# Optimization experiments

Hardware: AMD Instinct MI355X
Metric: run time of the kernel (lower is better)

The kernel has to match this reference:

```python
import jax, jax.numpy as jnp
import numpy as np

# Static config (matches init_kwargs)
B, F, CIN, COUT, H, W = 2, 8, 16, 32, 128, 128
RB, GB = 1, 1                 # refer_band, guard_band_dop (range_doppler)
KH, KW = 2 * (RB + GB), 4     # PeakConv kernel
N = KH * KW                   # ring samples per pixel (16)
LEAK, EPS = 0.01, 1e-5


def _ring_offsets(rb, gb):
    """Peripheral-reference-frame ring offsets, in the exact order of _gen_prf_grid."""
    r = rb + gb
    hp = 2 * r + 1
    xs, ys = np.meshgrid(np.arange(-r, r + 1), np.arange(-r, r + 1), indexing='ij')
    def ring(a):
        top = a[0:rb]
        rgt = a[rb:hp - 2 * rb + 1, hp - rb:hp]
        dwn = a[hp - rb:hp]
        lft = a[rb:hp - 2 * rb + 1, 0:rb]
        return np.concatenate([top.ravel(), rgt.ravel(), dwn.ravel(), lft.ravel()])
    return ring(xs), ring(ys)

_OX, _OY = _ring_offsets(RB, GB)  # each (N,)


def _peak_conv(x, Wk, bk):
    # x: (b, c, h, w)
    bsz, c, h, w = x.shape
    pad = RB + GB
    xp = jnp.pad(x, ((0, 0), (0, 0), (pad, pad), (pad, pad)))
    ii = jnp.arange(h)[:, None, None] + pad + jnp.asarray(_OX)[None, None, :]  # (h,1,N)
    jj = jnp.arange(w)[None, :, None] + pad + jnp.asarray(_OY)[None, None, :]  # (1,w,N)
    x_r = xp[:, :, ii, jj]                       # (b,c,h,w,N) ring gather
    diff = x[..., None] - x_r                    # center minus ring (x_c - x_r)
    diff = diff.reshape(bsz, c, h, w, KH, KW)    # matches _reshape_x_prf tiling
    # conv with kernel (KH,KW), stride (KH,KW) over tiled map == per-pixel contraction
    return jnp.einsum('bchwgj,ocgj->bohw', diff, Wk) + bk[None, :, None, None]


def _bn_leaky(x, gamma, beta):
    mu = x.mean(axis=(0, 2, 3), keepdims=True)
    var = x.var(axis=(0, 2, 3), keepdims=True)  # biased, as torch BN uses for normalization
    y = (x - mu) * jax.lax.rsqrt(var + EPS)
    y = y * gamma[None, :, None, None] + beta[None, :, None, None]
    return jnp.where(y >= 0, y, LEAK * y)


def setup_inputs() -> dict:
    key = jax.random.key(0)
    ks = jax.random.split(key, 5)
    return {
        'x':  jax.random.normal(ks[0], (B, CIN, F, H, W), dtype=jnp.float32),
        'W1': jax.random.normal(ks[1], (COUT, CIN, KH, KW), dtype=jnp.float32) * 0.05,
        'b1': jax.random.normal(ks[2], (COUT,), dtype=jnp.float32) * 0.05,
        'g1': jnp.ones((COUT,), jnp.float32),
        'be1': jnp.zeros((COUT,), jnp.float32),
        'W2': jax.random.normal(ks[3], (COUT, COUT, KH, KW), dtype=jnp.float32) * 0.05,
        'b2': jax.random.normal(ks[4], (COUT,), dtype=jnp.float32) * 0.05,
        'g2': jnp.ones((COUT,), jnp.float32),
        'be2': jnp.zeros((COUT,), jnp.float32),
    }


def reference(x, W1, b1, g1, be1, W2, b2, g2, be2):
    # (B, CIN, F, H, W) -> permute -> flatten to (B*F, CIN, H, W)
    xx = jnp.transpose(x, (0, 2, 1, 3, 4)).reshape(B * F, CIN, H, W)
    y = _bn_leaky(_peak_conv(xx, W1, b1), g1, be1)
    y = _bn_leaky(_peak_conv(y, W2, b2), g2, be2)
    # NOTE: original does .view(B, C, F, h, w) on a (B*F, C, h, w) contiguous
    # tensor — a raw reinterpretation, reproduced exactly by this reshape.
    y = y.reshape(B, COUT, F, H, W)
    return y.mean(axis=2, keepdims=True)  # AvgPool3d((F,1,1)) -> (B, COUT, 1, H, W)
```

## Files before the change

### kernel.cpp

```cpp
#include <hip/hip_runtime.h>

using short8 = __attribute__((ext_vector_type(8))) short;
using sh4    = __attribute__((ext_vector_type(4))) short;
using f32x4  = __attribute__((ext_vector_type(4))) float;
typedef unsigned short ushort_t;

constexpr int BB = 2, FF = 8, CIN = 16, COUT = 32, HH = 128, WW = 128;
constexpr int HW   = HH * WW;
constexpr int NIMG = BB * FF;
constexpr int TIL = 16, HALO = 2, LP = 20, NPX = 400;
constexpr int NSLOT = 1024;
constexpr int WFN = 17 * 2 * 512;

__device__ const int DOFF[17] = { -42,-41,-40,-39,-38, -18,2,22, 38,39,40,41,42, -22,-2,18, 0 };

__device__ __forceinline__ float leaky(float v) { return v >= 0.f ? v : 0.01f * v; }
__device__ __forceinline__ ushort_t f2bf(float f) {
    unsigned u = __builtin_bit_cast(unsigned, f);
    u = (u + 0x7FFFu + ((u >> 16) & 1u)) >> 16;
    return (ushort_t)u;
}
__device__ __forceinline__ float bf2f(ushort_t h) {
    unsigned u = ((unsigned)h) << 16;
    return __builtin_bit_cast(float, u);
}

__global__ __launch_bounds__(256)
void prep_weights(const float* __restrict__ W1, const float* __restrict__ W2,
                  ushort_t* __restrict__ Wf1, ushort_t* __restrict__ Wf2)
{
    int which = blockIdx.y;
    const float* W = which ? W2 : W1;
    ushort_t* Wf   = which ? Wf2 : Wf1;
    int ci         = which ? COUT : CIN;

    int idx = blockIdx.x * 256 + threadIdx.x;
    int j  = idx & 7;
    int l  = (idx >> 3) & 63;
    int oh = (idx >> 9) & 1;
    int n  = idx >> 10;
    int oc = oh * 16 + (l & 15);
    int k  = ((l >> 4) << 3) + j;
    int c  = which ? k : (k & 15);
    const float* wp = W + ((size_t)oc * ci + c) * 16;
    float v;
    if (n < 16) v = -wp[n];
    else { v = 0.f; for (int q = 0; q < 16; ++q) v += wp[q]; }
    Wf[idx] = f2bf(v);
}

template <int MODE>
__global__ __launch_bounds__(256)
void peak_conv_mfma(const float* __restrict__ inf, const ushort_t* __restrict__ inh,
                    const ushort_t* __restrict__ Wf,
                    const float* __restrict__ bk, const float* __restrict__ prm,
                    ushort_t* __restrict__ outp, float* __restrict__ P)
{
    __shared__ __align__(16) ushort_t lds[NPX * 32];
    __shared__ float redS[4][COUT], redQ[4][COUT];

    const int tid    = threadIdx.x;
    const int tileid = blockIdx.x;
    const int img    = blockIdx.y;
    const int tx     = (tileid & 7) * TIL;
    const int ty     = (tileid >> 3) * TIL;
    const int lane   = tid & 63;
    const int wid    = tid >> 6;
    const int rxl    = lane & 15;
    const int cq     = lane >> 4;

    if (MODE == 0) {
#pragma unroll
        for (int e = 0; e < 4; ++e) {
            int task = e * 256 + tid;
            if (task < 800) {
                int h  = task >= 400 ? 1 : 0;
                int p  = task - h * 400;
                int ry = p / LP, rx = p - ry * LP;
                int gh = ty + ry - HALO, gw = tx + rx - HALO;
                bool ok = (unsigned)gh < (unsigned)HH && (unsigned)gw < (unsigned)WW;
                int ghc = min(max(gh, 0), HH - 1), gwc = min(max(gw, 0), WW - 1);
                const float* base = inf + (((size_t)(img >> 3) * CIN + 8 * h) * FF + (img & 7)) * HW
                                       + ghc * WW + gwc;
                short8 hi8, lo8;
#pragma unroll
                for (int cc = 0; cc < 8; ++cc) {
                    float v = base[(size_t)cc * FF * HW];
                    v = ok ? v : 0.f;
                    ushort_t hi = f2bf(v);
                    hi8[cc] = (short)hi;
                    lo8[cc] = (short)f2bf(v - bf2f(hi));
                }
                int swz = (p & 3) ^ ((p >> 2) & 3);
                *(short8*)&lds[p * 32 + 8 * (h ^ swz)]       = hi8;
                *(short8*)&lds[p * 32 + 8 * ((2 + h) ^ swz)] = lo8;
            }
        }
    } else {
#pragma unroll
        for (int e = 0; e < 7; ++e) {
            int task = e * 256 + tid;
            if (task < 1600) {
                int g  = task & 3, p = task >> 2;
                int ry = p / LP, rx = p - ry * LP;
                int gh = ty + ry - HALO, gw = tx + rx - HALO;
                bool ok = (unsigned)gh < (unsigned)HH && (unsigned)gw < (unsigned)WW;
                int ghc = min(max(gh, 0), HH - 1), gwc = min(max(gw, 0), WW - 1);
                const ushort_t* px = inh + ((size_t)img * HW + ghc * WW + gwc) * 32 + 8 * g;
                short8 raw = *(const short8*)px;
                short8 hv;
#pragma unroll
                for (int jj = 0; jj < 8; ++jj) {
                    int c = 8 * g + jj;
                    float v = bf2f((ushort_t)raw[jj]);
                    v = leaky(fmaf(prm[c], v, prm[COUT + c]));
                    hv[jj] = (short)f2bf(ok ? v : 0.f);
                }
                int swz = (p & 3) ^ ((p >> 2) & 3);
                *(short8*)&lds[p * 32 + 8 * (g ^ swz)] = hv;
            }
        }
    }
    __syncthreads();

    f32x4 acc[4][2];
#pragma unroll
    for (int ng = 0; ng < 4; ++ng)
#pragma unroll
        for (int oh = 0; oh < 2; ++oh) acc[ng][oh] = f32x4{0.f, 0.f, 0.f, 0.f};

    int q0[4];
#pragma unroll
    for (int ng = 0; ng < 4; ++ng) q0[ng] = (wid * 4 + ng + HALO) * LP + (rxl + HALO);

    const ushort_t* wl = Wf + (size_t)lane * 8;

#pragma unroll 1
    for (int n = 0; n < 17; ++n) {
        short8 A0 = *(const short8*)(wl + (size_t)(n * 2 + 0) * 512);
        short8 A1 = *(const short8*)(wl + (size_t)(n * 2 + 1) * 512);
        int dof = DOFF[n];
#pragma unroll
        for (int ng = 0; ng < 4; ++ng) {
            int p   = q0[ng] + dof;
            int swz = (p & 3) ^ ((p >> 2) & 3);
            short8 Bv = *(const short8*)&lds[p * 32 + 8 * (cq ^ swz)];
            acc[ng][0] = __builtin_amdgcn_mfma_f32_16x16x32_bf16(A0, Bv, acc[ng][0], 0, 0, 0);
            acc[ng][1] = __builtin_amdgcn_mfma_f32_16x16x32_bf16(A1, Bv, acc[ng][1], 0, 0, 0);
        }
    }

    float bias_[2][4];
#pragma unroll
    for (int oh = 0; oh < 2; ++oh)
#pragma unroll
        for (int rr = 0; rr < 4; ++rr) bias_[oh][rr] = bk[oh * 16 + cq * 4 + rr];

    float ssum[2][4], ssq[2][4];
#pragma unroll
    for (int oh = 0; oh < 2; ++oh)
#pragma unroll
        for (int rr = 0; rr < 4; ++rr) { ssum[oh][rr] = 0.f; ssq[oh][rr] = 0.f; }

#pragma unroll
    for (int ng = 0; ng < 4; ++ng) {
        int gh = ty + wid * 4 + ng, gw = tx + rxl;
        size_t pxb = ((size_t)img * HW + gh * WW + gw) * 32;
#pragma unroll
        for (int oh = 0; oh < 2; ++oh) {
            sh4 sv;
#pragma unroll
            for (int rr = 0; rr < 4; ++rr) {
                float v = acc[ng][oh][rr] + bias_[oh][rr];
                sv[rr] = (short)f2bf(v);
                ssum[oh][rr] += v;
                ssq[oh][rr]   = fmaf(v, v, ssq[oh][rr]);
            }
            *(sh4*)&outp[pxb + oh * 16 + cq * 4] = sv;
        }
    }

#pragma unroll
    for (int oh = 0; oh < 2; ++oh)
#pragma unroll
        for (int rr = 0; rr < 4; ++rr) {
            float s = ssum[oh][rr], q = ssq[oh][rr];
#pragma unroll
            for (int m = 1; m < 16; m <<= 1) { s += __shfl_xor(s, m); q += __shfl_xor(q, m); }
            if (rxl == 0) {
                redS[wid][oh * 16 + cq * 4 + rr] = s;
                redQ[wid][oh * 16 + cq * 4 + rr] = q;
            }
        }
    __syncthreads();

    const int slot = img * 64 + tileid;
    if (tid < COUT) {
        float s = redS[0][tid] + redS[1][tid] + redS[2][tid] + redS[3][tid];
        P[(size_t)tid * NSLOT + slot] = s;
    } else if (tid < 2 * COUT) {
        int oc = tid - COUT;
        float q = redQ[0][oc] + redQ[1][oc] + redQ[2][oc] + redQ[3][oc];
        P[(size_t)COUT * NSLOT + (size_t)oc * NSLOT + slot] = q;
    }
}

__global__ __launch_bounds__(256)
void bn_stats(const float* __restrict__ P, const float* __restrict__ gamma,
              const float* __restrict__ beta, float* __restrict__ prm)
{
    __shared__ float rs[256], rq[256];
    const int c = blockIdx.x, tid = threadIdx.x;
    const float* Ps = P + (size_t)c * NSLOT;
    const float* Pq = P + (size_t)COUT * NSLOT + (size_t)c * NSLOT;
    rs[tid] = Ps[tid] + Ps[tid + 256] + Ps[tid + 512] + Ps[tid + 768];
    rq[tid] = Pq[tid] + Pq[tid + 256] + Pq[tid + 512] + Pq[tid + 768];
    __syncthreads();
    for (int s = 128; s > 0; s >>= 1) {
        if (tid < s) { rs[tid] += rs[tid + s]; rq[tid] += rq[tid + s]; }
        __syncthreads();
    }
    if (tid == 0) {
        const float n = (float)(NIMG * HW);
        float mu  = rs[0] / n;
        float var = rq[0] / n - mu * mu;
        float a   = gamma[c] * rsqrtf(var + 1e-5f);
        prm[c]        = a;
        prm[COUT + c] = beta[c] - mu * a;
    }
}

__global__ __launch_bounds__(256)
void finalize(const ushort_t* __restrict__ t2, const float* __restrict__ prm,
              float* __restrict__ outp)
{
    int gid  = blockIdx.x * 256 + threadIdx.x;
    int p    = gid & (HW - 1);
    int rest = gid >> 14;
    int o    = rest & 31;
    int b    = rest >> 5;
    int img  = b * 8 + (o >> 2);
    int cb   = (o & 3) * 8;
    const ushort_t* px = t2 + ((size_t)img * HW + p) * 32 + cb;
    short8 raw = *(const short8*)px;
    float s = 0.f;
#pragma unroll
    for (int j = 0; j < 8; ++j) {
        int c = cb + j;
        float v = bf2f((ushort_t)raw[j]);
        s += leaky(fmaf(prm[c], v, prm[COUT + c]));
    }
    outp[gid] = 0.125f * s;
}

extern "C" void kernel_launch(void* const* d_in, const int* in_sizes, int n_in,
                              void* d_out, int out_size, void* d_ws, size_t ws_size,
                              hipStream_t stream)
{
    const float* x   = (const float*)d_in[0];
    const float* W1  = (const float*)d_in[1];
    const float* b1  = (const float*)d_in[2];
    const float* g1  = (const float*)d_in[3];
    const float* be1 = (const float*)d_in[4];
    const float* W2  = (const float*)d_in[5];
    const float* b2  = (const float*)d_in[6];
    const float* g2  = (const float*)d_in[7];
    const float* be2 = (const float*)d_in[8];
    float* out = (float*)d_out;

    const size_t TSZH = (size_t)NIMG * HW * 32;
    ushort_t* t1   = (ushort_t*)d_ws;
    ushort_t* t2   = t1 + TSZH;
    float*    P    = (float*)(t2 + TSZH);
    float*    prm1 = P + 2 * COUT * NSLOT;
    float*    prm2 = prm1 + 2 * COUT;
    ushort_t* Wf1  = (ushort_t*)(prm2 + 2 * COUT);
    ushort_t* Wf2  = Wf1 + WFN;

    dim3 pg(WFN / 256, 2);
    prep_weights<<<pg, 256, 0, stream>>>(W1, W2, Wf1, Wf2);

    dim3 cg(64, NIMG);
    peak_conv_mfma<0><<<cg, 256, 0, stream>>>(x,  nullptr, Wf1, b1, nullptr, t1, P);
    bn_stats<<<COUT, 256, 0, stream>>>(P, g1, be1, prm1);
    peak_conv_mfma<1><<<cg, 256, 0, stream>>>(nullptr, t1, Wf2, b2, prm1,   t2, P);
    bn_stats<<<COUT, 256, 0, stream>>>(P, g2, be2, prm2);
    finalize<<<(BB * COUT * HW) / 256, 256, 0, stream>>>(t2, prm2, out);
}
```

Before: 64.18 us.

## Fuse whole pipeline into one cooperative kernel with grid syncs

Replaces the six-launch sequence (weight prep, two convs, two BN-stat reductions, finalize) with a single cooperative kernel that uses grid-wide syncs between phases. Each block does the BN statistics reduction redundantly, and the second conv's accumulators stay in registers for the final BN+leaky+frame-average, so the t2 intermediate is never written or re-read. Partial sums are stored interleaved as (sum, sumsq) pairs. The aim is to remove launch gaps and one round trip of the intermediate through memory, at the cost of grid-sync latency, redundant per-block reductions, and needing all 1024 blocks co-resident. A fallback multi-kernel path with BN reduction folded into the consumers is kept for when cooperative launch is unavailable.

```diff
diff --git a/kernel.cpp b/kernel.cpp
--- a/kernel.cpp
+++ b/kernel.cpp
@@ -1,8 +1,12 @@
 #include <hip/hip_runtime.h>
+#include <hip/hip_cooperative_groups.h>
+
+namespace cg = cooperative_groups;
 
 using short8 = __attribute__((ext_vector_type(8))) short;
 using sh4    = __attribute__((ext_vector_type(4))) short;
 using f32x4  = __attribute__((ext_vector_type(4))) float;
+using f32x2  = __attribute__((ext_vector_type(2))) float;
 typedef unsigned short ushort_t;
 
 constexpr int BB = 2, FF = 8, CIN = 16, COUT = 32, HH = 128, WW = 128;
@@ -25,6 +29,265 @@
     return __builtin_bit_cast(float, u);
 }
 
+__device__ __forceinline__ void bn_reduce(const float* __restrict__ Pv,
+                                          const float* __restrict__ gamma,
+                                          const float* __restrict__ beta,
+                                          float* sprm, int tid)
+{
+    int c = tid >> 3, l8 = tid & 7;
+    const f32x2* base = (const f32x2*)(Pv + (size_t)c * 2 * NSLOT);
+    float s = 0.f, q = 0.f;
+    for (int k = 0; k < 128; ++k) {
+        f32x2 v = base[l8 + (k << 3)];
+        s += v[0]; q += v[1];
+    }
+#pragma unroll
+    for (int m = 1; m < 8; m <<= 1) { s += __shfl_xor(s, m); q += __shfl_xor(q, m); }
+    if (l8 == 0) {
+        const float n = (float)(NIMG * HW);
+        float mu  = s / n;
+        float var = q / n - mu * mu;
+        float a   = gamma[c] * rsqrtf(var + 1e-5f);
+        sprm[c]        = a;
+        sprm[COUT + c] = beta[c] - mu * a;
+    }
+}
+
+template <int MODE, bool STORE>
+__device__ __forceinline__ void conv_phase(
+    const float* __restrict__ inf, const ushort_t* __restrict__ inh,
+    const ushort_t* __restrict__ Wf, const float* __restrict__ bk,
+    const float* sprm, ushort_t* __restrict__ tout, float* __restrict__ Pv,
+    ushort_t* lds, float (*redS)[COUT], float (*redQ)[COUT],
+    int img, int tileid, int tid, f32x4 (&acc)[4][2])
+{
+    const int tx   = (tileid & 7) * TIL;
+    const int ty   = (tileid >> 3) * TIL;
+    const int lane = tid & 63;
+    const int wid  = tid >> 6;
+    const int rxl  = lane & 15;
+    const int cq   = lane >> 4;
+
+    if (MODE == 0) {
+#pragma unroll
+        for (int e = 0; e < 4; ++e) {
+            int task = e * 256 + tid;
+            if (task < 800) {
+                int h  = task >= 400 ? 1 : 0;
+                int p  = task - h * 400;
+                int ry = p / LP, rx = p - ry * LP;
+                int gh = ty + ry - HALO, gw = tx + rx - HALO;
+                bool ok = (unsigned)gh < (unsigned)HH && (unsigned)gw < (unsigned)WW;
+                int ghc = min(max(gh, 0), HH - 1), gwc = min(max(gw, 0), WW - 1);
+                const float* base = inf + (((size_t)(img >> 3) * CIN + 8 * h) * FF + (img & 7)) * HW
+                                       + ghc * WW + gwc;
+                short8 hi8, lo8;
+#pragma unroll
+                for (int cc = 0; cc < 8; ++cc) {
+                    float v = base[(size_t)cc * FF * HW];
+                    v = ok ? v : 0.f;
+                    ushort_t hi = f2bf(v);
+                    hi8[cc] = (short)hi;
+                    lo8[cc] = (short)f2bf(v - bf2f(hi));
+                }
+                int swz = (p & 3) ^ ((p >> 2) & 3);
+                *(short8*)&lds[p * 32 + 8 * (h ^ swz)]       = hi8;
+                *(short8*)&lds[p * 32 + 8 * ((2 + h) ^ swz)] = lo8;
+            }
+        }
+    } else {
+#pragma unroll
+        for (int e = 0; e < 7; ++e) {
+            int task = e * 256 + tid;
+            if (task < 1600) {
+                int g  = task & 3, p = task >> 2;
+                int ry = p / LP, rx = p - ry * LP;
+                int gh = ty + ry - HALO, gw = tx + rx - HALO;
+                bool ok = (unsigned)gh < (unsigned)HH && (unsigned)gw < (unsigned)WW;
+                int ghc = min(max(gh, 0), HH - 1), gwc = min(max(gw, 0), WW - 1);
+                const ushort_t* px = inh + ((size_t)img * HW + ghc * WW + gwc) * 32 + 8 * g;
+                short8 raw = *(const short8*)px;
+                short8 hv;
+#pragma unroll
+                for (int jj = 0; jj < 8; ++jj) {
+                    int c = 8 * g + jj;
+                    float v = bf2f((ushort_t)raw[jj]);
+                    v = leaky(fmaf(sprm[c], v, sprm[COUT + c]));
+                    hv[jj] = (short)f2bf(ok ? v : 0.f);
+                }
+                int swz = (p & 3) ^ ((p >> 2) & 3);
+                *(short8*)&lds[p * 32 + 8 * (g ^ swz)] = hv;
+            }
+        }
+    }
+    __syncthreads();
+
+#pragma unroll
+    for (int ng = 0; ng < 4; ++ng)
+#pragma unroll
+        for (int oh = 0; oh < 2; ++oh) acc[ng][oh] = f32x4{0.f, 0.f, 0.f, 0.f};
+
+    int q0[4];
+#pragma unroll
+    for (int ng = 0; ng < 4; ++ng) q0[ng] = (wid * 4 + ng + HALO) * LP + (rxl + HALO);
+
+    const ushort_t* wl = Wf + (size_t)lane * 8;
+
+#pragma unroll 1
+    for (int n = 0; n < 17; ++n) {
+        short8 A0 = *(const short8*)(wl + (size_t)(n * 2 + 0) * 512);
+        short8 A1 = *(const short8*)(wl + (size_t)(n * 2 + 1) * 512);
+        int dof = DOFF[n];
+#pragma unroll
+        for (int ng = 0; ng < 4; ++ng) {
+            int p   = q0[ng] + dof;
+            int swz = (p & 3) ^ ((p >> 2) & 3);
+            short8 Bv = *(const short8*)&lds[p * 32 + 8 * (cq ^ swz)];
+            acc[ng][0] = __builtin_amdgcn_mfma_f32_16x16x32_bf16(A0, Bv, acc[ng][0], 0, 0, 0);
+            acc[ng][1] = __builtin_amdgcn_mfma_f32_16x16x32_bf16(A1, Bv, acc[ng][1], 0, 0, 0);
+        }
+    }
+
+    float ssum[2][4], ssq[2][4];
+#pragma unroll
+    for (int oh = 0; oh < 2; ++oh)
+#pragma unroll
+        for (int rr = 0; rr < 4; ++rr) {
+            float b = bk[oh * 16 + cq * 4 + rr];
+#pragma unroll
+            for (int ng = 0; ng < 4; ++ng) acc[ng][oh][rr] += b;
+            ssum[oh][rr] = 0.f; ssq[oh][rr] = 0.f;
+        }
+
+#pragma unroll
+    for (int ng = 0; ng < 4; ++ng) {
+        int gh = ty + wid * 4 + ng, gw = tx + rxl;
+        size_t pxb = ((size_t)img * HW + gh * WW + gw) * 32;
+#pragma unroll
+        for (int oh = 0; oh < 2; ++oh) {
+            sh4 sv;
+#pragma unroll
+            for (int rr = 0; rr < 4; ++rr) {
+                float v = acc[ng][oh][rr];
+                sv[rr] = (short)f2bf(v);
+                ssum[oh][rr] += v;
+                ssq[oh][rr]   = fmaf(v, v, ssq[oh][rr]);
+            }
+            if (STORE) *(sh4*)&tout[pxb + oh * 16 + cq * 4] = sv;
+        }
+    }
+
+#pragma unroll
+    for (int oh = 0; oh < 2; ++oh)
+#pragma unroll
+        for (int rr = 0; rr < 4; ++rr) {
+            float s = ssum[oh][rr], q = ssq[oh][rr];
+#pragma unroll
+            for (int m = 1; m < 16; m <<= 1) { s += __shfl_xor(s, m); q += __shfl_xor(q, m); }
+            if (rxl == 0) {
+                redS[wid][oh * 16 + cq * 4 + rr] = s;
+                redQ[wid][oh * 16 + cq * 4 + rr] = q;
+            }
+        }
+    __syncthreads();
+
+    const int slot = img * 64 + tileid;
+    if (tid < COUT) {
+        float s = redS[0][tid] + redS[1][tid] + redS[2][tid] + redS[3][tid];
+        float q = redQ[0][tid] + redQ[1][tid] + redQ[2][tid] + redQ[3][tid];
+        ((f32x2*)Pv)[(size_t)tid * NSLOT + slot] = f32x2{s, q};
+    }
+}
+
+__global__ __launch_bounds__(256, 4)
+void fused(const float* __restrict__ x,  const float* __restrict__ W1,
+           const float* __restrict__ b1, const float* __restrict__ g1,
+           const float* __restrict__ be1, const float* __restrict__ W2,
+           const float* __restrict__ b2, const float* __restrict__ g2,
+           const float* __restrict__ be2, float* __restrict__ out,
+           ushort_t* __restrict__ t1, float* __restrict__ Pv1,
+           float* __restrict__ Pv2, ushort_t* __restrict__ Wf1,
+           ushort_t* __restrict__ Wf2)
+{
+    cg::grid_group grid = cg::this_grid();
+
+    __shared__ __align__(16) ushort_t lds[NPX * 32];
+    __shared__ float redS[4][COUT], redQ[4][COUT];
+    __shared__ float sprm[2 * COUT];
+
+    const int tid    = threadIdx.x;
+    const int tileid = blockIdx.x;
+    const int img    = blockIdx.y;
+    const int bid    = img * 64 + tileid;
+
+    if (bid < 2 * WFN / 256) {
+        int idx   = bid * 256 + tid;
+        int which = idx >= WFN;
+        int sub   = which ? idx - WFN : idx;
+        const float* W = which ? W2 : W1;
+        ushort_t* Wf   = which ? Wf2 : Wf1;
+        int ci         = which ? COUT : CIN;
+        int j  = sub & 7;
+        int l  = (sub >> 3) & 63;
+        int oh = (sub >> 9) & 1;
+        int n  = sub >> 10;
+        int oc = oh * 16 + (l & 15);
+        int k  = ((l >> 4) << 3) + j;
+        int c  = which ? k : (k & 15);
+        const float* wp = W + ((size_t)oc * ci + c) * 16;
+        float v;
+        if (n < 16) v = -wp[n];
+        else { v = 0.f; for (int q = 0; q < 16; ++q) v += wp[q]; }
+        Wf[sub] = f2bf(v);
+    }
+    __threadfence();
+    grid.sync();
+    __threadfence();
+
+    f32x4 acc[4][2];
+    conv_phase<0, true>(x, nullptr, Wf1, b1, nullptr, t1, Pv1,
+                        lds, redS, redQ, img, tileid, tid, acc);
+    __threadfence();
+    grid.sync();
+    __threadfence();
+
+    bn_reduce(Pv1, g1, be1, sprm, tid);
+    __syncthreads();
+
+    conv_phase<1, false>(nullptr, t1, Wf2, b2, sprm, nullptr, Pv2,
+                         lds, redS, redQ, img, tileid, tid, acc);
+    __threadfence();
+    grid.sync();
+    __threadfence();
+
+    bn_reduce(Pv2, g2, be2, sprm, tid);
+    __syncthreads();
+
+    const int lane = tid & 63, wid = tid >> 6;
+    const int rxl  = lane & 15, cq = lane >> 4;
+    const int tx   = (tileid & 7) * TIL, ty = (tileid >> 3) * TIL;
+    const int b    = img >> 3;
+    const int obase = (img & 7) * 4;
+#pragma unroll
+    for (int ng = 0; ng < 4; ++ng) {
+        int gh = ty + wid * 4 + ng, gw = tx + rxl;
+#pragma unroll
+        for (int oh = 0; oh < 2; ++oh) {
+            float s = 0.f;
+#pragma unroll
+            for (int rr = 0; rr < 4; ++rr) {
+                int c = oh * 16 + cq * 4 + rr;
+                s += leaky(fmaf(sprm[c], acc[ng][oh][rr], sprm[COUT + c]));
+            }
+            s += __shfl_xor(s, 16);
+            if ((cq & 1) == 0) {
+                int o = obase + oh * 2 + (cq >> 1);
+                out[((size_t)b * COUT + o) * HW + gh * WW + gw] = 0.125f * s;
+            }
+        }
+    }
+}
+
 __global__ __launch_bounds__(256)
 void prep_weights(const float* __restrict__ W1, const float* __restrict__ W2,
                   ushort_t* __restrict__ Wf1, ushort_t* __restrict__ Wf2)
@@ -33,7 +296,6 @@
     const float* W = which ? W2 : W1;
     ushort_t* Wf   = which ? Wf2 : Wf1;
     int ci         = which ? COUT : CIN;
-
     int idx = blockIdx.x * 256 + threadIdx.x;
     int j  = idx & 7;
     int l  = (idx >> 3) & 63;
@@ -49,208 +311,63 @@
     Wf[idx] = f2bf(v);
 }
 
-template <int MODE>
 __global__ __launch_bounds__(256)
-void peak_conv_mfma(const float* __restrict__ inf, const ushort_t* __restrict__ inh,
-                    const ushort_t* __restrict__ Wf,
-                    const float* __restrict__ bk, const float* __restrict__ prm,
-                    ushort_t* __restrict__ outp, float* __restrict__ P)
+void conv1_k(const float* __restrict__ x, const ushort_t* __restrict__ Wf1,
+             const float* __restrict__ b1, ushort_t* __restrict__ t1,
+             float* __restrict__ Pv1)
 {
     __shared__ __align__(16) ushort_t lds[NPX * 32];
     __shared__ float redS[4][COUT], redQ[4][COUT];
-
-    const int tid    = threadIdx.x;
-    const int tileid = blockIdx.x;
-    const int img    = blockIdx.y;
-    const int tx     = (tileid & 7) * TIL;
-    const int ty     = (tileid >> 3) * TIL;
-    const int lane   = tid & 63;
-    const int wid    = tid >> 6;
-    const int rxl    = lane & 15;
-    const int cq     = lane >> 4;
-
-    if (MODE == 0) {
-#pragma unroll
-        for (int e = 0; e < 4; ++e) {
-            int task = e * 256 + tid;
-            if (task < 800) {
-                int h  = task >= 400 ? 1 : 0;
-                int p  = task - h * 400;
-                int ry = p / LP, rx = p - ry * LP;
-                int gh = ty + ry - HALO, gw = tx + rx - HALO;
-                bool ok = (unsigned)gh < (unsigned)HH && (unsigned)gw < (unsigned)WW;
-                int ghc = min(max(gh, 0), HH - 1), gwc = min(max(gw, 0), WW - 1);
-                const float* base = inf + (((size_t)(img >> 3) * CIN + 8 * h) * FF + (img & 7)) * HW
-                                       + ghc * WW + gwc;
-                short8 hi8, lo8;
-#pragma unroll
-                for (int cc = 0; cc < 8; ++cc) {
-                    float v = base[(size_t)cc * FF * HW];
-                    v = ok ? v : 0.f;
-                    ushort_t hi = f2bf(v);
-                    hi8[cc] = (short)hi;
-                    lo8[cc] = (short)f2bf(v - bf2f(hi));
-                }
-                int swz = (p & 3) ^ ((p >> 2) & 3);
-                *(short8*)&lds[p * 32 + 8 * (h ^ swz)]       = hi8;
-                *(short8*)&lds[p * 32 + 8 * ((2 + h) ^ swz)] = lo8;
-            }
-        }
-    } else {
-#pragma unroll
-        for (int e = 0; e < 7; ++e) {
-            int task = e * 256 + tid;
-            if (task < 1600) {
-                int g  = task & 3, p = task >> 2;
-                int ry = p / LP, rx = p - ry * LP;
-                int gh = ty + ry - HALO, gw = tx + rx - HALO;
-                bool ok = (unsigned)gh < (unsigned)HH && (unsigned)gw < (unsigned)WW;
-                int ghc = min(max(gh, 0), HH - 1), gwc = min(max(gw, 0), WW - 1);
-                const ushort_t* px = inh + ((size_t)img * HW + ghc * WW + gwc) * 32 + 8 * g;
-                short8 raw = *(const short8*)px;
-                short8 hv;
-#pragma unroll
-                for (int jj = 0; jj < 8; ++jj) {
-                    int c = 8 * g + jj;
-                    float v = bf2f((ushort_t)raw[jj]);
-                    v = leaky(fmaf(prm[c], v, prm[COUT + c]));
-                    hv[jj] = (short)f2bf(ok ? v : 0.f);
-                }
-                int swz = (p & 3) ^ ((p >> 2) & 3);
-                *(short8*)&lds[p * 32 + 8 * (g ^ swz)] = hv;
-            }
-        }
-    }
-    __syncthreads();
-
     f32x4 acc[4][2];
-#pragma unroll
-    for (int ng = 0; ng < 4; ++ng)
-#pragma unroll
-        for (int oh = 0; oh < 2; ++oh) acc[ng][oh] = f32x4{0.f, 0.f, 0.f, 0.f};
-
-    int q0[4];
-#pragma unroll
-    for (int ng = 0; ng < 4; ++ng) q0[ng] = (wid * 4 + ng + HALO) * LP + (rxl + HALO);
-
-    const ushort_t* wl = Wf + (size_t)lane * 8;
-
-#pragma unroll 1
-    for (int n = 0; n < 17; ++n) {
-        short8 A0 = *(const short8*)(wl + (size_t)(n * 2 + 0) * 512);
-        short8 A1 = *(const short8*)(wl + (size_t)(n * 2 + 1) * 512);
-        int dof = DOFF[n];
-#pragma unroll
-        for (int ng = 0; ng < 4; ++ng) {
-            int p   = q0[ng] + dof;
-            int swz = (p & 3) ^ ((p >> 2) & 3);
-            short8 Bv = *(const short8*)&lds[p * 32 + 8 * (cq ^ swz)];
-            acc[ng][0] = __builtin_amdgcn_mfma_f32_16x16x32_bf16(A0, Bv, acc[ng][0], 0, 0, 0);
-            acc[ng][1] = __builtin_amdgcn_mfma_f32_16x16x32_bf16(A1, Bv, acc[ng][1], 0, 0, 0);
-        }
-    }
-
-    float bias_[2][4];
-#pragma unroll
-    for (int oh = 0; oh < 2; ++oh)
-#pragma unroll
-        for (int rr = 0; rr < 4; ++rr) bias_[oh][rr] = bk[oh * 16 + cq * 4 + rr];
-
-    float ssum[2][4], ssq[2][4];
-#pragma unroll
-    for (int oh = 0; oh < 2; ++oh)
-#pragma unroll
-        for (int rr = 0; rr < 4; ++rr) { ssum[oh][rr] = 0.f; ssq[oh][rr] = 0.f; }
-
-#pragma unroll
-    for (int ng = 0; ng < 4; ++ng) {
-        int gh = ty + wid * 4 + ng, gw = tx + rxl;
-        size_t pxb = ((size_t)img * HW + gh * WW + gw) * 32;
-#pragma unroll
-        for (int oh = 0; oh < 2; ++oh) {
-            sh4 sv;
-#pragma unroll
-            for (int rr = 0; rr < 4; ++rr) {
-                float v = acc[ng][oh][rr] + bias_[oh][rr];
-                sv[rr] = (short)f2bf(v);
-                ssum[oh][rr] += v;
-                ssq[oh][rr]   = fmaf(v, v, ssq[oh][rr]);
-            }
-            *(sh4*)&outp[pxb + oh * 16 + cq * 4] = sv;
-        }
-    }
-
-#pragma unroll
-    for (int oh = 0; oh < 2; ++oh)
-#pragma unroll
-        for (int rr = 0; rr < 4; ++rr) {
-            float s = ssum[oh][rr], q = ssq[oh][rr];
-#pragma unroll
-            for (int m = 1; m < 16; m <<= 1) { s += __shfl_xor(s, m); q += __shfl_xor(q, m); }
-            if (rxl == 0) {
-                redS[wid][oh * 16 + cq * 4 + rr] = s;
-                redQ[wid][oh * 16 + cq * 4 + rr] = q;
-            }
-        }
-    __syncthreads();
-
-    const int slot = img * 64 + tileid;
-    if (tid < COUT) {
-        float s = redS[0][tid] + redS[1][tid] + redS[2][tid] + redS[3][tid];
-        P[(size_t)tid * NSLOT + slot] = s;
-    } else if (tid < 2 * COUT) {
-        int oc = tid - COUT;
-        float q = redQ[0][oc] + redQ[1][oc] + redQ[2][oc] + redQ[3][oc];
-        P[(size_t)COUT * NSLOT + (size_t)oc * NSLOT + slot] = q;
-    }
+    conv_phase<0, true>(x, nullptr, Wf1, b1, nullptr, t1, Pv1,
+                        lds, redS, redQ, blockIdx.y, blockIdx.x, threadIdx.x, acc);
 }
 
 __global__ __launch_bounds__(256)
-void bn_stats(const float* __restrict__ P, const float* __restrict__ gamma,
-              const float* __restrict__ beta, float* __restrict__ prm)
-{
-    __shared__ float rs[256], rq[256];
-    const int c = blockIdx.x, tid = threadIdx.x;
-    const float* Ps = P + (size_t)c * NSLOT;
-    const float* Pq = P + (size_t)COUT * NSLOT + (size_t)c * NSLOT;
-    rs[tid] = Ps[tid] + Ps[tid + 256] + Ps[tid + 512] + Ps[tid + 768];
-    rq[tid] = Pq[tid] + Pq[tid + 256] + Pq[tid + 512] + Pq[tid + 768];
-    __syncthreads();
-    for (int s = 128; s > 0; s >>= 1) {
-        if (tid < s) { rs[tid] += rs[tid + s]; rq[tid] += rq[tid + s]; }
-        __syncthreads();
-    }
-    if (tid == 0) {
-        const float n = (float)(NIMG * HW);
-        float mu  = rs[0] / n;
-        float var = rq[0] / n - mu * mu;
-        float a   = gamma[c] * rsqrtf(var + 1e-5f);
-        prm[c]        = a;
-        prm[COUT + c] = beta[c] - mu * a;
-    }
+void conv2_k(const ushort_t* __restrict__ t1, const ushort_t* __restrict__ Wf2,
+             const float* __restrict__ b2, const float* __restrict__ Pv1,
+             const float* __restrict__ g1, const float* __restrict__ be1,
+             ushort_t* __restrict__ t2, float* __restrict__ Pv2)
+{
+    __shared__ __align__(16) ushort_t lds[NPX * 32];
+    __shared__ float redS[4][COUT], redQ[4][COUT];
+    __shared__ float sprm[2 * COUT];
+    bn_reduce(Pv1, g1, be1, sprm, threadIdx.x);
+    __syncthreads();
+    f32x4 acc[4][2];
+    conv_phase<1, true>(nullptr, t1, Wf2, b2, sprm, t2, Pv2,
+                        lds, redS, redQ, blockIdx.y, blockIdx.x, threadIdx.x, acc);
 }
 
 __global__ __launch_bounds__(256)
-void finalize(const ushort_t* __restrict__ t2, const float* __restrict__ prm,
-              float* __restrict__ outp)
-{
-    int gid  = blockIdx.x * 256 + threadIdx.x;
-    int p    = gid & (HW - 1);
-    int rest = gid >> 14;
-    int o    = rest & 31;
-    int b    = rest >> 5;
-    int img  = b * 8 + (o >> 2);
-    int cb   = (o & 3) * 8;
-    const ushort_t* px = t2 + ((size_t)img * HW + p) * 32 + cb;
-    short8 raw = *(const short8*)px;
-    float s = 0.f;
-#pragma unroll
-    for (int j = 0; j < 8; ++j) {
-        int c = cb + j;
-        float v = bf2f((ushort_t)raw[j]);
-        s += leaky(fmaf(prm[c], v, prm[COUT + c]));
-    }
-    outp[gid] = 0.125f * s;
+void finalize_k(const ushort_t* __restrict__ t2, const float* __restrict__ Pv2,
+                const float* __restrict__ g2, const float* __restrict__ be2,
+                float* __restrict__ outp)
+{
+    __shared__ float sprm[2 * COUT];
+    bn_reduce(Pv2, g2, be2, sprm, threadIdx.x);
+    __syncthreads();
+    int base = blockIdx.x * 1024;
+#pragma unroll
+    for (int e = 0; e < 4; ++e) {
+        int gid  = base + e * 256 + threadIdx.x;
+        int p    = gid & (HW - 1);
+        int rest = gid >> 14;
+        int o    = rest & 31;
+        int b    = rest >> 5;
+        int img  = b * 8 + (o >> 2);
+        int cb   = (o & 3) * 8;
+        const ushort_t* px = t2 + ((size_t)img * HW + p) * 32 + cb;
+        short8 raw = *(const short8*)px;
+        float s = 0.f;
+#pragma unroll
+        for (int j = 0; j < 8; ++j) {
+            int c = cb + j;
+            float v = bf2f((ushort_t)raw[j]);
+            s += leaky(fmaf(sprm[c], v, sprm[COUT + c]));
+        }
+        outp[gid] = 0.125f * s;
+    }
 }
 
 extern "C" void kernel_launch(void* const* d_in, const int* in_sizes, int n_in,
@@ -271,19 +388,34 @@
     const size_t TSZH = (size_t)NIMG * HW * 32;
     ushort_t* t1   = (ushort_t*)d_ws;
     ushort_t* t2   = t1 + TSZH;
-    float*    P    = (float*)(t2 + TSZH);
-    float*    prm1 = P + 2 * COUT * NSLOT;
-    float*    prm2 = prm1 + 2 * COUT;
-    ushort_t* Wf1  = (ushort_t*)(prm2 + 2 * COUT);
+    float*    Pv1  = (float*)(t2 + TSZH);
+    float*    Pv2  = Pv1 + 2 * COUT * NSLOT;
+    ushort_t* Wf1  = (ushort_t*)(Pv2 + 2 * COUT * NSLOT);
     ushort_t* Wf2  = Wf1 + WFN;
 
-    dim3 pg(WFN / 256, 2);
-    prep_weights<<<pg, 256, 0, stream>>>(W1, W2, Wf1, Wf2);
-
-    dim3 cg(64, NIMG);
-    peak_conv_mfma<0><<<cg, 256, 0, stream>>>(x,  nullptr, Wf1, b1, nullptr, t1, P);
-    bn_stats<<<COUT, 256, 0, stream>>>(P, g1, be1, prm1);
-    peak_conv_mfma<1><<<cg, 256, 0, stream>>>(nullptr, t1, Wf2, b2, prm1,   t2, P);
-    bn_stats<<<COUT, 256, 0, stream>>>(P, g2, be2, prm2);
-    finalize<<<(BB * COUT * HW) / 256, 256, 0, stream>>>(t2, prm2, out);
-}
+    int dev = 0;
+    hipGetDevice(&dev);
+    int coopAttr = 0;
+    hipDeviceGetAttribute(&coopAttr, hipDeviceAttributeCooperativeLaunch, dev);
+    int maxB = 0;
+    hipOccupancyMaxActiveBlocksPerMultiprocessor(&maxB, (const void*)fused, 256, 0);
+
+    bool coop_done = false;
+    if (coopAttr && maxB >= 4) {
+        void* args[] = { (void*)&x,  (void*)&W1, (void*)&b1, (void*)&g1, (void*)&be1,
+                         (void*)&W2, (void*)&b2, (void*)&g2, (void*)&be2,
+                         (void*)&out, (void*)&t1, (void*)&Pv1, (void*)&Pv2,
+                         (void*)&Wf1, (void*)&Wf2 };
+        hipError_t e = hipLaunchCooperativeKernel((const void*)fused, dim3(64, NIMG),
+                                                  dim3(256), args, 0, stream);
+        coop_done = (e == hipSuccess);
+    }
+    if (!coop_done) {
+        dim3 pg(WFN / 256, 2);
+        prep_weights<<<pg, 256, 0, stream>>>(W1, W2, Wf1, Wf2);
+        dim3 cg_(64, NIMG);
+        conv1_k<<<cg_, 256, 0, stream>>>(x, Wf1, b1, t1, Pv1);
+        conv2_k<<<cg_, 256, 0, stream>>>(t1, Wf2, b2, Pv1, g1, be1, t2, Pv2);
+        finalize_k<<<(BB * COUT * HW) / 1024, 256, 0, stream>>>(t2, Pv2, g2, be2, out);
+    }
+}
```

Result: slower. 82.74 us (+28.9%).
